# Optimization experiments

Hardware: AMD Instinct MI355X
Metric: run time of the kernel (lower is better)

Reference implementation:

```python
import jax, jax.numpy as jnp
import numpy as np

N_A, N_B = 50000, 10000
E = 300000
IN_F, HID, BEL_OUT, INC_OUT = 256, 256, 128, 128


def _gconv(x_src, W, b, src, dst, n_src, n_dst):
    """DGL GraphConv with norm='both': D_in^{-1/2} A D_out^{-1/2} X W + b, degs clamped to >=1."""
    ones = jnp.ones(src.shape[0], x_src.dtype)
    deg_out = jnp.maximum(jax.ops.segment_sum(ones, src, num_segments=n_src), 1.0)
    deg_in = jnp.maximum(jax.ops.segment_sum(ones, dst, num_segments=n_dst), 1.0)
    h = (x_src * jax.lax.rsqrt(deg_out)[:, None]) @ W        # [n_src, out]
    agg = jax.ops.segment_sum(h[src], dst, num_segments=n_dst)  # scatter-add messages
    return agg * jax.lax.rsqrt(deg_in)[:, None] + b


def setup_inputs() -> dict:
    key = jax.random.key(0)
    ks = jax.random.split(key, 12)
    s = 1.0 / np.sqrt(IN_F)
    sh = 1.0 / np.sqrt(HID)
    return {
        "x_a": jax.random.normal(ks[0], (N_A, IN_F), jnp.float32),
        "x_b": jax.random.normal(ks[1], (N_B, IN_F), jnp.float32),
        "W1_bel": jax.random.normal(ks[2], (IN_F, HID), jnp.float32) * s,
        "b1_bel": jnp.zeros((HID,), jnp.float32),
        "W1_inc": jax.random.normal(ks[3], (IN_F, HID), jnp.float32) * s,
        "b1_inc": jnp.zeros((HID,), jnp.float32),
        "W2_bel": jax.random.normal(ks[4], (HID, BEL_OUT), jnp.float32) * sh,
        "b2_bel": jnp.zeros((BEL_OUT,), jnp.float32),
        "W2_inc": jax.random.normal(ks[5], (HID, INC_OUT), jnp.float32) * sh,
        "b2_inc": jnp.zeros((INC_OUT,), jnp.float32),
        "bel_src": jax.random.randint(ks[6], (E,), 0, N_A, jnp.int32),
        "bel_dst": jax.random.randint(ks[7], (E,), 0, N_B, jnp.int32),
        "inc_src": jax.random.randint(ks[8], (E,), 0, N_B, jnp.int32),
        "inc_dst": jax.random.randint(ks[9], (E,), 0, N_A, jnp.int32),
    }


def reference(x_a, x_b, W1_bel, b1_bel, W1_inc, b1_inc, W2_bel, b2_bel,
              W2_inc, b2_inc, bel_src, bel_dst, inc_src, inc_dst):
    n_a, n_b = x_a.shape[0], x_b.shape[0]
    # layer 1 (HeteroGraphConv, mean over a single relation per dst type = identity)
    h_b = _gconv(x_a, W1_bel, b1_bel, bel_src, bel_dst, n_a, n_b)  # 'belongs_to': A->B
    h_a = _gconv(x_b, W1_inc, b1_inc, inc_src, inc_dst, n_b, n_a)  # 'including' : B->A
    h_a = jax.nn.relu(h_a)
    h_b = jax.nn.relu(h_b)
    # layer 2
    out_b = _gconv(h_a, W2_bel, b2_bel, bel_src, bel_dst, n_a, n_b)  # [N_B, bel_out]
    out_a = _gconv(h_b, W2_inc, b2_inc, inc_src, inc_dst, n_b, n_a)  # [N_A, inc_out]
    return out_a, out_b
```

## Files before the change

kernel.cpp:

```cpp
#include <hip/hip_runtime.h>


#define NA 50000
#define NB 10000
#define NE 300000
#define GB 625
#define HB 1172
#define PB 64
#define CB 300
#define CS 32

typedef unsigned short u16;
typedef unsigned int u32;
typedef __attribute__((ext_vector_type(8))) short short8;
typedef __attribute__((ext_vector_type(4))) float f32x4;
typedef __attribute__((ext_vector_type(2))) float f32x2;
typedef __attribute__((ext_vector_type(4))) unsigned short u16x4;
typedef __attribute__((ext_vector_type(4))) int i32x4;

__device__ __forceinline__ float bf2f(u16 h){
  union { u32 u; float f; } x; x.u = ((u32)h) << 16; return x.f;
}
__device__ __forceinline__ u16 f2bf(float f){
  union { float f; u32 u; } x; x.f = f;
  u32 r = (x.u + 0x7FFFu + ((x.u >> 16) & 1u)) >> 16;
  return (u16)r;
}

__device__ __forceinline__ void pack_elem(int t,
    const float* __restrict__ W1b, const float* __restrict__ W1i,
    const float* __restrict__ W2b, const float* __restrict__ W2i,
    u16* __restrict__ pwh, u16* __restrict__ pwl){
  const float* W; int N; int tt;
  if (t < 65536)       { W = W1b; N = 256; tt = t; }
  else if (t < 131072) { W = W1i; N = 256; tt = t - 65536; }
  else if (t < 163840) { W = W2b; N = 128; tt = t - 131072; }
  else                 { W = W2i; N = 128; tt = t - 163840; }
  int j = tt & 7, lane = (tt >> 3) & 63, tile = tt >> 9;
  int nT = N >> 4;
  int nt = tile % nT, kt = tile / nT;
  int k = kt * 32 + ((lane >> 4) << 3) + j;
  int n = nt * 16 + (lane & 15);
  float v = W[k * N + n];
  u16 hi = f2bf(v);
  pwh[t] = hi;
  pwl[t] = f2bf(v - bf2f(hi));
}

__global__ __launch_bounds__(256) void pre_kernel(
    int* __restrict__ z, int nz4, const float* __restrict__ W1i,
    u16* __restrict__ pwh, u16* __restrict__ pwl){
  int g = blockIdx.x * blockDim.x + threadIdx.x;
  int s = gridDim.x * blockDim.x;
  i32x4* z4 = (i32x4*)z;
  i32x4 zero = {0, 0, 0, 0};
  for (int i = g; i < nz4; i += s) __builtin_nontemporal_store(zero, z4 + i);
  for (int t = g; t < 65536; t += s)
    pack_elem(65536 + t, nullptr, W1i, nullptr, nullptr, pwh, pwl);
}

__device__ __forceinline__ void gemm_dev(int blk, const float* __restrict__ A,
                                         const u16* __restrict__ PWH,
                                         const u16* __restrict__ PWL,
                                         const float* __restrict__ bias,
                                         const float* __restrict__ rs,
                                         float* __restrict__ Cf,
                                         u16* __restrict__ C16,
                                         int M, int nT, int wpsShift,
                                         int doRelu, int ldC, int colOff){
  int wave = blk * 4 + (threadIdx.x >> 6);
  int lane = threadIdx.x & 63;
  int strips = M >> 4;
  int strip = wave >> wpsShift;
  if (strip >= strips) return;
  int slice = wave & ((1 << wpsShift) - 1);
  int ntPer = nT >> wpsShift;
  int ntStart = slice * ntPer;
  int r16 = lane & 15, quad = lane >> 4;
  int m0 = strip << 4;
  const float* aBase = A + (size_t)(m0 + r16) * 256 + quad * 8;
  short8 ah[8], al[8];
#pragma unroll
  for (int kt = 0; kt < 8; ++kt){
    float4 p0 = *(const float4*)(aBase + kt * 32);
    float4 p1 = *(const float4*)(aBase + kt * 32 + 4);
    float v[8] = {p0.x, p0.y, p0.z, p0.w, p1.x, p1.y, p1.z, p1.w};
    short8 h, l;
#pragma unroll
    for (int j = 0; j < 8; ++j){
      u16 hb = f2bf(v[j]);
      h[j] = (short)hb;
      l[j] = (short)f2bf(v[j] - bf2f(hb));
    }
    ah[kt] = h; al[kt] = l;
  }
  float rscale[4];
#pragma unroll
  for (int r = 0; r < 4; ++r) rscale[r] = rs ? rs[m0 + quad * 4 + r] : 1.f;
  for (int nt = ntStart; nt < ntStart + ntPer; ++nt){
    f32x4 acc = {0.f, 0.f, 0.f, 0.f};
    const u16* bh = PWH + ((size_t)nt * 64 + lane) * 8;
    const u16* bl = PWL + ((size_t)nt * 64 + lane) * 8;
#pragma unroll
    for (int kt = 0; kt < 8; ++kt){
      short8 wh = *(const short8*)(bh + (size_t)kt * nT * 512);
      short8 wl = *(const short8*)(bl + (size_t)kt * nT * 512);
      acc = __builtin_amdgcn_mfma_f32_16x16x32_bf16(ah[kt], wh, acc, 0, 0, 0);
      acc = __builtin_amdgcn_mfma_f32_16x16x32_bf16(al[kt], wh, acc, 0, 0, 0);
      acc = __builtin_amdgcn_mfma_f32_16x16x32_bf16(ah[kt], wl, acc, 0, 0, 0);
    }
    int col = nt * 16 + r16;
    float bv = bias ? bias[col] : 0.f;
#pragma unroll
    for (int r = 0; r < 4; ++r){
      float v = acc[r] * rscale[r] + bv;
      if (doRelu) v = fmaxf(v, 0.f);
      size_t o = (size_t)(m0 + quad * 4 + r) * ldC + colOff + col;
      if (C16) __builtin_nontemporal_store(f2bf(v), C16 + o);
      else     __builtin_nontemporal_store(v, Cf + o);
    }
  }
}

__global__ __launch_bounds__(256) void mega_kernel(
    const float* __restrict__ xb,
    const u16* __restrict__ WH1i, const u16* __restrict__ WL1i,
    u16* __restrict__ G12,
    const int* __restrict__ bs, const int* __restrict__ bd,
    const int* __restrict__ isc, const int* __restrict__ idt,
    int* __restrict__ c_bs, int* __restrict__ c_bd,
    int* __restrict__ c_is, int* __restrict__ c_id,
    int* __restrict__ rank_bel, int* __restrict__ rank_inc,
    const float* __restrict__ W1b, const float* __restrict__ W2b,
    const float* __restrict__ W2i,
    u16* __restrict__ pwh, u16* __restrict__ pwl,
    const float* __restrict__ xa, u16* __restrict__ xa16){
  int blk = blockIdx.x;
  if (blk < GB){
    gemm_dev(blk, xb, WH1i, WL1i, nullptr, nullptr,
             nullptr, G12, NB, 16, 2, 0, 384, 0);
  } else if (blk < GB + HB){
    int g = (blk - GB) * blockDim.x + threadIdx.x;
    int s = HB * blockDim.x;
    for (int e = g; e < NE; e += s){
      atomicAdd(&c_bs[bs[e] * CS], 1);
      rank_bel[e] = atomicAdd(&c_bd[bd[e] * CS], 1);
      atomicAdd(&c_is[isc[e] * CS], 1);
      rank_inc[e] = atomicAdd(&c_id[idt[e] * CS], 1);
    }
  } else if (blk < GB + HB + PB){
    int g = (blk - GB - HB) * blockDim.x + threadIdx.x;
    int s = PB * blockDim.x;
    for (int v = g; v < 131072; v += s){
      int t = v < 65536 ? v : v + 65536;
      pack_elem(t, W1b, nullptr, W2b, W2i, pwh, pwl);
    }
  } else {
    int g = ((blk - GB - HB - PB) * blockDim.x + threadIdx.x) * 4;
    int s = CB * blockDim.x * 4;
    for (int i = g; i < NA * 256; i += s){
      float4 v = *(const float4*)(xa + i);
      u16x4 o;
      o.x = f2bf(v.x); o.y = f2bf(v.y); o.z = f2bf(v.z); o.w = f2bf(v.w);
      __builtin_nontemporal_store(o, (u16x4*)(xa16 + i));
    }
  }
}

template<int SEG>
__device__ __forceinline__ void scan_block(const int* __restrict__ cnt,
                                           int* __restrict__ off, int n){
  __shared__ int wsum[16];
  int tid = threadIdx.x, lane = tid & 63, wid = tid >> 6;
  int i0 = tid * SEG;
  int v[SEG];
#pragma unroll
  for (int r = 0; r < SEG; ++r){
    int idx = i0 + r;
    v[r] = (idx < n) ? cnt[idx * CS] : 0;
  }
  int sum = 0;
#pragma unroll
  for (int r = 0; r < SEG; ++r) sum += v[r];
  int x = sum;
#pragma unroll
  for (int d = 1; d < 64; d <<= 1){
    int t = __shfl_up(x, d, 64);
    if (lane >= d) x += t;
  }
  if (lane == 63) wsum[wid] = x;
  __syncthreads();
  if (wid == 0){
    int ws = (lane < 16) ? wsum[lane] : 0;
#pragma unroll
    for (int d = 1; d < 16; d <<= 1){
      int t = __shfl_up(ws, d, 64);
      if (lane >= d) ws += t;
    }
    if (lane < 16) wsum[lane] = ws;
  }
  __syncthreads();
  int run = (wid ? wsum[wid - 1] : 0) + (x - sum);
#pragma unroll
  for (int r = 0; r < SEG; ++r){
    int idx = i0 + r;
    if (idx < n) off[idx] = run;
    run += v[r];
  }
  if (tid == 0) off[n] = wsum[15];
}

__global__ __launch_bounds__(1024) void scan_scales_kernel(
    const int* __restrict__ c_bs, const int* __restrict__ c_bd,
    const int* __restrict__ c_is, const int* __restrict__ c_id,
    int* __restrict__ off_bel, int* __restrict__ off_inc,
    float* __restrict__ s_ob, float* __restrict__ s_ib,
    float* __restrict__ s_oi, float* __restrict__ s_ii){
  if (blockIdx.x >= 2){
    int g = (blockIdx.x - 2) * blockDim.x + threadIdx.x;
    int s = (gridDim.x - 2) * blockDim.x;
    for (int i = g; i < NA; i += s){
      int a = c_bs[i * CS]; s_ob[i] = rsqrtf((float)(a > 1 ? a : 1));
      int b = c_id[i * CS]; s_ii[i] = rsqrtf((float)(b > 1 ? b : 1));
      if (i < NB){
        int c = c_bd[i * CS]; s_ib[i] = rsqrtf((float)(c > 1 ? c : 1));
        int d = c_is[i * CS]; s_oi[i] = rsqrtf((float)(d > 1 ? d : 1));
      }
    }
    return;
  }
  if (blockIdx.x == 0) scan_block<10>(c_bd, off_bel, NB);
  else                 scan_block<49>(c_id, off_inc, NA);
}

__global__ __launch_bounds__(256) void fill_kernel(
    const int* __restrict__ bs, const int* __restrict__ bd,
    const int* __restrict__ isc, const int* __restrict__ idt,
    const int* __restrict__ rank_bel, const int* __restrict__ rank_inc,
    const int* __restrict__ off_bel, const int* __restrict__ off_inc,
    int* __restrict__ csr_bel, int* __restrict__ csr_inc){
  int g = blockIdx.x * blockDim.x + threadIdx.x;
  int s = gridDim.x * blockDim.x;
  for (int e = g; e < NE; e += s){
    csr_bel[off_bel[bd[e]] + rank_bel[e]] = bs[e];
    csr_inc[off_inc[idt[e]] + rank_inc[e]] = isc[e];
  }
}

__global__ __launch_bounds__(256) void agg_bel_kernel(
    const u16* __restrict__ X, const float* __restrict__ ss,
    const int* __restrict__ off, const int* __restrict__ csr,
    float* __restrict__ Pf, int nDst){
  int wave = blockIdx.x * 4 + (threadIdx.x >> 6);
  int lane = threadIdx.x & 63;
  if (wave >= nDst) return;
  int b0 = off[wave], b1 = off[wave + 1];
  int deg = b1 - b0;
  int part = lane >> 5;
  int cl = lane & 31;
  int c = cl * 8;
  float acc[8];
#pragma unroll
  for (int q = 0; q < 8; ++q) acc[q] = 0.f;
  int idx = 0; float sc = 0.f;
  if (lane < deg){
    idx = csr[b0 + lane];
    sc = ss ? ss[idx] : 1.f;
  }
  int lim = deg < 64 ? deg : 64;
  for (int u = 0; u < lim; u += 8){
    const u16* addr[4]; float w[4];
#pragma unroll
    for (int k = 0; k < 4; ++k){
      int e = u + k * 2 + part;
      int t = e < lim ? e : 0;
      int s0 = __shfl(idx, t, 64);
      float c0 = __shfl(sc, t, 64);
      w[k] = e < lim ? c0 : 0.f;
      addr[k] = X + (size_t)s0 * 256 + c;
    }
    short8 v[4];
#pragma unroll
    for (int k = 0; k < 4; ++k) v[k] = *(const short8*)addr[k];
#pragma unroll
    for (int k = 0; k < 4; ++k)
#pragma unroll
      for (int q = 0; q < 8; ++q) acc[q] += bf2f((u16)v[k][q]) * w[k];
  }
  for (int j = b0 + 64 + part; j < b1; j += 2){
    int s0 = csr[j];
    float c0 = ss ? ss[s0] : 1.f;
    short8 v0 = *(const short8*)(X + (size_t)s0 * 256 + c);
#pragma unroll
    for (int q = 0; q < 8; ++q) acc[q] += bf2f((u16)v0[q]) * c0;
  }
#pragma unroll
  for (int q = 0; q < 8; ++q) acc[q] += __shfl_xor(acc[q], 32, 64);
  if (part == 0){
    f32x4 f0 = {acc[0], acc[1], acc[2], acc[3]};
    f32x4 f1 = {acc[4], acc[5], acc[6], acc[7]};
    __builtin_nontemporal_store(f0, (f32x4*)(Pf + (size_t)wave * 256 + c));
    __builtin_nontemporal_store(f1, (f32x4*)(Pf + (size_t)wave * 256 + c + 4));
  }
}

__global__ __launch_bounds__(256) void gemmHG_kernel(
    const float* __restrict__ Pb,
    const u16* __restrict__ WH1b, const u16* __restrict__ WL1b,
    const float* __restrict__ b1b, const float* __restrict__ s_ib,
    const u16* __restrict__ WH2i, const u16* __restrict__ WL2i,
    u16* __restrict__ G12){
  __shared__ float Hs[16][260];
  int w = threadIdx.x >> 6;
  int lane = threadIdx.x & 63;
  int r16 = lane & 15, quad = lane >> 4;
  int m0 = blockIdx.x << 4;
  const float* aBase = Pb + (size_t)(m0 + r16) * 256 + quad * 8;
  short8 ah[8], al[8];
#pragma unroll
  for (int kt = 0; kt < 8; ++kt){
    float4 p0 = *(const float4*)(aBase + kt * 32);
    float4 p1 = *(const float4*)(aBase + kt * 32 + 4);
    float v[8] = {p0.x, p0.y, p0.z, p0.w, p1.x, p1.y, p1.z, p1.w};
    short8 h, l;
#pragma unroll
    for (int j = 0; j < 8; ++j){
      u16 hb = f2bf(v[j]);
      h[j] = (short)hb;
      l[j] = (short)f2bf(v[j] - bf2f(hb));
    }
    ah[kt] = h; al[kt] = l;
  }
  float rs1[4];
#pragma unroll
  for (int r = 0; r < 4; ++r) rs1[r] = s_ib[m0 + quad * 4 + r];
  for (int nt = w * 4; nt < w * 4 + 4; ++nt){
    f32x4 acc = {0.f, 0.f, 0.f, 0.f};
    const u16* bh = WH1b + ((size_t)nt * 64 + lane) * 8;
    const u16* bl = WL1b + ((size_t)nt * 64 + lane) * 8;
#pragma unroll
    for (int kt = 0; kt < 8; ++kt){
      short8 wh = *(const short8*)(bh + (size_t)kt * 16 * 512);
      short8 wl = *(const short8*)(bl + (size_t)kt * 16 * 512);
      acc = __builtin_amdgcn_mfma_f32_16x16x32_bf16(ah[kt], wh, acc, 0, 0, 0);
      acc = __builtin_amdgcn_mfma_f32_16x16x32_bf16(al[kt], wh, acc, 0, 0, 0);
      acc = __builtin_amdgcn_mfma_f32_16x16x32_bf16(ah[kt], wl, acc, 0, 0, 0);
    }
    int col = nt * 16 + r16;
    float bv = b1b[col];
#pragma unroll
    for (int r = 0; r < 4; ++r)
      Hs[quad * 4 + r][col] = fmaxf(acc[r] * rs1[r] + bv, 0.f);
  }
  __syncthreads();
  short8 ah2[8], al2[8];
#pragma unroll
  for (int kt = 0; kt < 8; ++kt){
    float4 p0 = *(const float4*)&Hs[r16][kt * 32 + quad * 8];
    float4 p1 = *(const float4*)&Hs[r16][kt * 32 + quad * 8 + 4];
    float v[8] = {p0.x, p0.y, p0.z, p0.w, p1.x, p1.y, p1.z, p1.w};
    short8 h, l;
#pragma unroll
    for (int j = 0; j < 8; ++j){
      u16 hb = f2bf(v[j]);
      h[j] = (short)hb;
      l[j] = (short)f2bf(v[j] - bf2f(hb));
    }
    ah2[kt] = h; al2[kt] = l;
  }
  for (int nt = w * 2; nt < w * 2 + 2; ++nt){
    f32x4 acc = {0.f, 0.f, 0.f, 0.f};
    const u16* bh = WH2i + ((size_t)nt * 64 + lane) * 8;
    const u16* bl = WL2i + ((size_t)nt * 64 + lane) * 8;
#pragma unroll
    for (int kt = 0; kt < 8; ++kt){
      short8 wh = *(const short8*)(bh + (size_t)kt * 8 * 512);
      short8 wl = *(const short8*)(bl + (size_t)kt * 8 * 512);
      acc = __builtin_amdgcn_mfma_f32_16x16x32_bf16(ah2[kt], wh, acc, 0, 0, 0);
      acc = __builtin_amdgcn_mfma_f32_16x16x32_bf16(al2[kt], wh, acc, 0, 0, 0);
      acc = __builtin_amdgcn_mfma_f32_16x16x32_bf16(ah2[kt], wl, acc, 0, 0, 0);
    }
    int col = nt * 16 + r16;
#pragma unroll
    for (int r = 0; r < 4; ++r){
      u16 o = f2bf(acc[r]);
      __builtin_nontemporal_store(o, G12 + (size_t)(m0 + quad * 4 + r) * 384 + 256 + col);
    }
  }
}

__global__ __launch_bounds__(256) void agg_inc2_kernel(
    const u16* __restrict__ G12, const int* __restrict__ off,
    const int* __restrict__ csr, const float* __restrict__ s_oi,
    const float* __restrict__ s_ii, const float* __restrict__ s_ob,
    const float* __restrict__ b1i, const float* __restrict__ b2i,
    u16* __restrict__ Ha, float* __restrict__ outa){
  int wave = blockIdx.x * 4 + (threadIdx.x >> 6);
  int lane = threadIdx.x & 63;
  if (wave >= NA) return;
  int b0 = off[wave], b1 = off[wave + 1];
  int deg = b1 - b0;
  int c1 = lane * 4;
  int c2 = lane * 2;
  float acc[6];
#pragma unroll
  for (int q = 0; q < 6; ++q) acc[q] = 0.f;
  int idx = 0; float sc = 0.f;
  if (lane < deg){
    idx = csr[b0 + lane];
    sc = s_oi[idx];
  }
  int lim = deg < 64 ? deg : 64;
  for (int u = 0; u < lim; u += 4){
    ushort4 va[4]; ushort2 vb[4]; float w[4];
#pragma unroll
    for (int k = 0; k < 4; ++k){
      int e = u + k;
      int t = e < lim ? e : 0;
      int se = __shfl(idx, t, 64);
      float c0 = __shfl(sc, t, 64);
      w[k] = e < lim ? c0 : 0.f;
      const u16* r = G12 + (size_t)se * 384;
      va[k] = *(const ushort4*)(r + c1);
      vb[k] = *(const ushort2*)(r + 256 + c2);
    }
#pragma unroll
    for (int k = 0; k < 4; ++k){
      acc[0] += bf2f(va[k].x) * w[k];
      acc[1] += bf2f(va[k].y) * w[k];
      acc[2] += bf2f(va[k].z) * w[k];
      acc[3] += bf2f(va[k].w) * w[k];
      acc[4] += bf2f(vb[k].x) * w[k];
      acc[5] += bf2f(vb[k].y) * w[k];
    }
  }
  for (int j = b0 + 64; j < b1; ++j){
    int se = csr[j];
    float c0 = s_oi[se];
    const u16* r = G12 + (size_t)se * 384;
    ushort4 va = *(const ushort4*)(r + c1);
    ushort2 vb = *(const ushort2*)(r + 256 + c2);
    acc[0] += bf2f(va.x) * c0; acc[1] += bf2f(va.y) * c0;
    acc[2] += bf2f(va.z) * c0; acc[3] += bf2f(va.w) * c0;
    acc[4] += bf2f(vb.x) * c0; acc[5] += bf2f(vb.y) * c0;
  }
  float sii = s_ii[wave], sob = s_ob[wave];
  float4 bb1 = *(const float4*)(b1i + c1);
  f32x2 bb2 = *(const f32x2*)(b2i + c2);
  u16x4 o1;
  o1.x = f2bf(fmaxf(acc[0] * sii + bb1.x, 0.f) * sob);
  o1.y = f2bf(fmaxf(acc[1] * sii + bb1.y, 0.f) * sob);
  o1.z = f2bf(fmaxf(acc[2] * sii + bb1.z, 0.f) * sob);
  o1.w = f2bf(fmaxf(acc[3] * sii + bb1.w, 0.f) * sob);
  __builtin_nontemporal_store(o1, (u16x4*)(Ha + (size_t)wave * 256 + c1));
  f32x2 o2 = {acc[4] * sii + bb2.x, acc[5] * sii + bb2.y};
  __builtin_nontemporal_store(o2, (f32x2*)(outa + (size_t)wave * 128 + c2));
}

__global__ __launch_bounds__(256) void gemm_kernel(
    const float* __restrict__ A,
    const u16* __restrict__ PWH, const u16* __restrict__ PWL,
    const float* __restrict__ bias, const float* __restrict__ rs,
    float* __restrict__ Cf, u16* __restrict__ C16,
    int M, int nT, int wpsShift, int doRelu, int ldC, int colOff){
  gemm_dev(blockIdx.x, A, PWH, PWL, bias, rs, Cf, C16,
           M, nT, wpsShift, doRelu, ldC, colOff);
}

extern "C" void kernel_launch(void* const* d_in, const int* in_sizes, int n_in,
                              void* d_out, int out_size, void* d_ws, size_t ws_size,
                              hipStream_t stream){
  const float* x_a = (const float*)d_in[0];
  const float* x_b = (const float*)d_in[1];
  const float* W1b = (const float*)d_in[2];
  const float* b1b = (const float*)d_in[3];
  const float* W1i = (const float*)d_in[4];
  const float* b1i = (const float*)d_in[5];
  const float* W2b = (const float*)d_in[6];
  const float* b2b = (const float*)d_in[7];
  const float* W2i = (const float*)d_in[8];
  const float* b2i = (const float*)d_in[9];
  const int* bs  = (const int*)d_in[10];
  const int* bd  = (const int*)d_in[11];
  const int* isc = (const int*)d_in[12];
  const int* idt = (const int*)d_in[13];

  char* w = (char*)d_ws;
  size_t o = 0;
  auto take = [&](size_t bytes) -> void* {
    void* p = w + o; o = (o + bytes + 255) & ~(size_t)255; return p;
  };
  int* zint = (int*)take((size_t)120000 * CS * sizeof(int));
  int* c_bs = zint;
  int* c_bd = zint + (size_t)50000 * CS;
  int* c_is = zint + (size_t)60000 * CS;
  int* c_id = zint + (size_t)70000 * CS;
  int* rank_bel = (int*)take(NE * sizeof(int));
  int* rank_inc = (int*)take(NE * sizeof(int));
  int* off_bel = (int*)take((NB + 1) * sizeof(int));
  int* off_inc = (int*)take((NA + 1) * sizeof(int));
  int* csr_bel = (int*)take(NE * sizeof(int));
  int* csr_inc = (int*)take(NE * sizeof(int));
  float* s_ob = (float*)take(NA * sizeof(float));
  float* s_ib = (float*)take(NB * sizeof(float));
  float* s_oi = (float*)take(NB * sizeof(float));
  float* s_ii = (float*)take(NA * sizeof(float));
  u16* pwh = (u16*)take(196608 * sizeof(u16));
  u16* pwl = (u16*)take(196608 * sizeof(u16));
  u16* pwh1b = pwh, *pwh1i = pwh + 65536, *pwh2b = pwh + 131072, *pwh2i = pwh + 163840;
  u16* pwl1b = pwl, *pwl1i = pwl + 65536, *pwl2b = pwl + 131072, *pwl2i = pwl + 163840;
  u16* xa16 = (u16*)take((size_t)NA * 256 * sizeof(u16));
  u16* G12  = (u16*)take((size_t)NB * 384 * sizeof(u16));
  u16* H_a  = (u16*)take((size_t)NA * 256 * sizeof(u16));
  float* P_b = (float*)take((size_t)NB * 256 * sizeof(float));

  float* out_a = (float*)d_out;
  float* out_b = (float*)d_out + (size_t)NA * 128;

  pre_kernel<<<512, 256, 0, stream>>>(zint, 120000 * CS / 4, W1i, pwh, pwl);
  mega_kernel<<<GB + HB + PB + CB, 256, 0, stream>>>(
      x_b, pwh1i, pwl1i, G12,
      bs, bd, isc, idt, c_bs, c_bd, c_is, c_id, rank_bel, rank_inc,
      W1b, W2b, W2i, pwh, pwl, x_a, xa16);
  scan_scales_kernel<<<52, 1024, 0, stream>>>(c_bs, c_bd, c_is, c_id,
                                              off_bel, off_inc,
                                              s_ob, s_ib, s_oi, s_ii);
  fill_kernel<<<1172, 256, 0, stream>>>(bs, bd, isc, idt, rank_bel, rank_inc,
                                        off_bel, off_inc, csr_bel, csr_inc);
  agg_bel_kernel<<<2500, 256, 0, stream>>>(xa16, s_ob, off_bel, csr_bel, P_b, NB);
  gemmHG_kernel<<<625, 256, 0, stream>>>(P_b, pwh1b, pwl1b, b1b, s_ib,
                                         pwh2i, pwl2i, G12);
  agg_inc2_kernel<<<12500, 256, 0, stream>>>(G12, off_inc, csr_inc, s_oi,
                                             s_ii, s_ob, b1i, b2i, H_a, out_a);
  agg_bel_kernel<<<2500, 256, 0, stream>>>(H_a, nullptr, off_bel, csr_bel, P_b, NB);
  gemm_kernel<<<625, 256, 0, stream>>>(P_b, pwh2b, pwl2b, b2b, s_ib,
                                       out_b, nullptr, NB, 8, 2, 0, 128, 0);
}
```

Measured before the change: 401.0 us.

## Replace padded degree counters with compact and 4-way split counters

Drops the 32-int padding per degree counter, which had each counter sit on its own cache line, so the zeroing pass and the counter reads touch far less memory. For the small node sets (10k B nodes), the counters become four sub-counters per node picked by edge index, which spreads atomic contention, and the scan runs over 40000 entries so CSR offsets still stay correct. The large sets use dense unpadded counters. Denser counters risk more same-line atomic contention, and the bel scan now does more work per thread.

New measurement: 363.5 us. 9.4% less time.

```diff
diff --git a/kernel.cpp b/kernel.cpp
--- a/kernel.cpp
+++ b/kernel.cpp
@@ -8,7 +8,6 @@
 #define HB 1172
 #define PB 64
 #define CB 300
-#define CS 32
 
 typedef unsigned short u16;
 typedef unsigned int u32;
@@ -128,8 +127,8 @@
     u16* __restrict__ G12,
     const int* __restrict__ bs, const int* __restrict__ bd,
     const int* __restrict__ isc, const int* __restrict__ idt,
-    int* __restrict__ c_bs, int* __restrict__ c_bd,
-    int* __restrict__ c_is, int* __restrict__ c_id,
+    int* __restrict__ c_bs, int* __restrict__ c_bd4,
+    int* __restrict__ c_is4, int* __restrict__ c_id,
     int* __restrict__ rank_bel, int* __restrict__ rank_inc,
     const float* __restrict__ W1b, const float* __restrict__ W2b,
     const float* __restrict__ W2i,
@@ -143,10 +142,11 @@
     int g = (blk - GB) * blockDim.x + threadIdx.x;
     int s = HB * blockDim.x;
     for (int e = g; e < NE; e += s){
-      atomicAdd(&c_bs[bs[e] * CS], 1);
-      rank_bel[e] = atomicAdd(&c_bd[bd[e] * CS], 1);
-      atomicAdd(&c_is[isc[e] * CS], 1);
-      rank_inc[e] = atomicAdd(&c_id[idt[e] * CS], 1);
+      int r = e & 3;
+      atomicAdd(&c_bs[bs[e]], 1);
+      rank_bel[e] = atomicAdd(&c_bd4[bd[e] * 4 + r], 1);
+      atomicAdd(&c_is4[isc[e] * 4 + r], 1);
+      rank_inc[e] = atomicAdd(&c_id[idt[e]], 1);
     }
   } else if (blk < GB + HB + PB){
     int g = (blk - GB - HB) * blockDim.x + threadIdx.x;
@@ -177,7 +177,7 @@
 #pragma unroll
   for (int r = 0; r < SEG; ++r){
     int idx = i0 + r;
-    v[r] = (idx < n) ? cnt[idx * CS] : 0;
+    v[r] = (idx < n) ? cnt[idx] : 0;
   }
   int sum = 0;
 #pragma unroll
@@ -211,25 +211,29 @@
 }
 
 __global__ __launch_bounds__(1024) void scan_scales_kernel(
-    const int* __restrict__ c_bs, const int* __restrict__ c_bd,
-    const int* __restrict__ c_is, const int* __restrict__ c_id,
-    int* __restrict__ off_bel, int* __restrict__ off_inc,
+    const int* __restrict__ c_bs, const int* __restrict__ c_bd4,
+    const int* __restrict__ c_is4, const int* __restrict__ c_id,
+    int* __restrict__ off_bel4, int* __restrict__ off_inc,
     float* __restrict__ s_ob, float* __restrict__ s_ib,
     float* __restrict__ s_oi, float* __restrict__ s_ii){
   if (blockIdx.x >= 2){
     int g = (blockIdx.x - 2) * blockDim.x + threadIdx.x;
     int s = (gridDim.x - 2) * blockDim.x;
     for (int i = g; i < NA; i += s){
-      int a = c_bs[i * CS]; s_ob[i] = rsqrtf((float)(a > 1 ? a : 1));
-      int b = c_id[i * CS]; s_ii[i] = rsqrtf((float)(b > 1 ? b : 1));
+      int a = c_bs[i]; s_ob[i] = rsqrtf((float)(a > 1 ? a : 1));
+      int b = c_id[i]; s_ii[i] = rsqrtf((float)(b > 1 ? b : 1));
       if (i < NB){
-        int c = c_bd[i * CS]; s_ib[i] = rsqrtf((float)(c > 1 ? c : 1));
-        int d = c_is[i * CS]; s_oi[i] = rsqrtf((float)(d > 1 ? d : 1));
+        i32x4 cb = *(const i32x4*)(c_bd4 + i * 4);
+        int c = cb[0] + cb[1] + cb[2] + cb[3];
+        s_ib[i] = rsqrtf((float)(c > 1 ? c : 1));
+        i32x4 ci = *(const i32x4*)(c_is4 + i * 4);
+        int d = ci[0] + ci[1] + ci[2] + ci[3];
+        s_oi[i] = rsqrtf((float)(d > 1 ? d : 1));
       }
     }
     return;
   }
-  if (blockIdx.x == 0) scan_block<10>(c_bd, off_bel, NB);
+  if (blockIdx.x == 0) scan_block<40>(c_bd4, off_bel4, 40000);
   else                 scan_block<49>(c_id, off_inc, NA);
 }
 
@@ -237,24 +241,25 @@
     const int* __restrict__ bs, const int* __restrict__ bd,
     const int* __restrict__ isc, const int* __restrict__ idt,
     const int* __restrict__ rank_bel, const int* __restrict__ rank_inc,
-    const int* __restrict__ off_bel, const int* __restrict__ off_inc,
+    const int* __restrict__ off_bel4, const int* __restrict__ off_inc,
     int* __restrict__ csr_bel, int* __restrict__ csr_inc){
   int g = blockIdx.x * blockDim.x + threadIdx.x;
   int s = gridDim.x * blockDim.x;
   for (int e = g; e < NE; e += s){
-    csr_bel[off_bel[bd[e]] + rank_bel[e]] = bs[e];
+    int r = e & 3;
+    csr_bel[off_bel4[bd[e] * 4 + r] + rank_bel[e]] = bs[e];
     csr_inc[off_inc[idt[e]] + rank_inc[e]] = isc[e];
   }
 }
 
 __global__ __launch_bounds__(256) void agg_bel_kernel(
     const u16* __restrict__ X, const float* __restrict__ ss,
-    const int* __restrict__ off, const int* __restrict__ csr,
+    const int* __restrict__ off4, const int* __restrict__ csr,
     float* __restrict__ Pf, int nDst){
   int wave = blockIdx.x * 4 + (threadIdx.x >> 6);
   int lane = threadIdx.x & 63;
   if (wave >= nDst) return;
-  int b0 = off[wave], b1 = off[wave + 1];
+  int b0 = off4[wave * 4], b1 = off4[wave * 4 + 4];
   int deg = b1 - b0;
   int part = lane >> 5;
   int cl = lane & 31;
@@ -490,15 +495,15 @@
   auto take = [&](size_t bytes) -> void* {
     void* p = w + o; o = (o + bytes + 255) & ~(size_t)255; return p;
   };
-  int* zint = (int*)take((size_t)120000 * CS * sizeof(int));
-  int* c_bs = zint;
-  int* c_bd = zint + (size_t)50000 * CS;
-  int* c_is = zint + (size_t)60000 * CS;
-  int* c_id = zint + (size_t)70000 * CS;
+  int* zint = (int*)take((size_t)180000 * sizeof(int));
+  int* c_bs  = zint;
+  int* c_bd4 = zint + 50000;
+  int* c_is4 = zint + 90000;
+  int* c_id  = zint + 130000;
   int* rank_bel = (int*)take(NE * sizeof(int));
   int* rank_inc = (int*)take(NE * sizeof(int));
-  int* off_bel = (int*)take((NB + 1) * sizeof(int));
-  int* off_inc = (int*)take((NA + 1) * sizeof(int));
+  int* off_bel4 = (int*)take((40000 + 1) * sizeof(int));
+  int* off_inc  = (int*)take((NA + 1) * sizeof(int));
   int* csr_bel = (int*)take(NE * sizeof(int));
   int* csr_inc = (int*)take(NE * sizeof(int));
   float* s_ob = (float*)take(NA * sizeof(float));
@@ -517,22 +522,22 @@
   float* out_a = (float*)d_out;
   float* out_b = (float*)d_out + (size_t)NA * 128;
 
-  pre_kernel<<<512, 256, 0, stream>>>(zint, 120000 * CS / 4, W1i, pwh, pwl);
+  pre_kernel<<<256, 256, 0, stream>>>(zint, 180000 / 4, W1i, pwh, pwl);
   mega_kernel<<<GB + HB + PB + CB, 256, 0, stream>>>(
       x_b, pwh1i, pwl1i, G12,
-      bs, bd, isc, idt, c_bs, c_bd, c_is, c_id, rank_bel, rank_inc,
+      bs, bd, isc, idt, c_bs, c_bd4, c_is4, c_id, rank_bel, rank_inc,
       W1b, W2b, W2i, pwh, pwl, x_a, xa16);
-  scan_scales_kernel<<<52, 1024, 0, stream>>>(c_bs, c_bd, c_is, c_id,
-                                              off_bel, off_inc,
+  scan_scales_kernel<<<52, 1024, 0, stream>>>(c_bs, c_bd4, c_is4, c_id,
+                                              off_bel4, off_inc,
                                               s_ob, s_ib, s_oi, s_ii);
   fill_kernel<<<1172, 256, 0, stream>>>(bs, bd, isc, idt, rank_bel, rank_inc,
-                                        off_bel, off_inc, csr_bel, csr_inc);
-  agg_bel_kernel<<<2500, 256, 0, stream>>>(xa16, s_ob, off_bel, csr_bel, P_b, NB);
+                                        off_bel4, off_inc, csr_bel, csr_inc);
+  agg_bel_kernel<<<2500, 256, 0, stream>>>(xa16, s_ob, off_bel4, csr_bel, P_b, NB);
   gemmHG_kernel<<<625, 256, 0, stream>>>(P_b, pwh1b, pwl1b, b1b, s_ib,
                                          pwh2i, pwl2i, G12);
   agg_inc2_kernel<<<12500, 256, 0, stream>>>(G12, off_inc, csr_inc, s_oi,
                                              s_ii, s_ob, b1i, b2i, H_a, out_a);
-  agg_bel_kernel<<<2500, 256, 0, stream>>>(H_a, nullptr, off_bel, csr_bel, P_b, NB);
+  agg_bel_kernel<<<2500, 256, 0, stream>>>(H_a, nullptr, off_bel4, csr_bel, P_b, NB);
   gemm_kernel<<<625, 256, 0, stream>>>(P_b, pwh2b, pwl2b, b2b, s_ib,
                                        out_b, nullptr, NB, 8, 2, 0, 128, 0);
 }
```

## Replace global atomic degree counting with bin-partitioned LDS histograms

Applied to the files above, without the earlier changes.

Degree counting and CSR fill now use per-block shared-memory histograms. Each block owns a contiguous range of bins and scans the whole edge array, counting only edges whose endpoint falls in its range. Counts are written directly, so the padded counters, their zeroing pass and the per-edge rank arrays are no longer needed. Global atomics are replaced by LDS atomics, but each block now rereads all edges: 16x per array for counting and 32x per array in the fill, across only 64 blocks. With so few blocks the CSR fill may also be less parallel than before.

Result: slower. 709.3 us (+76.9%).

```diff
diff --git a/kernel.cpp b/kernel.cpp
--- a/kernel.cpp
+++ b/kernel.cpp
@@ -5,10 +5,9 @@
 #define NB 10000
 #define NE 300000
 #define GB 625
-#define HB 1172
+#define HBIN 64
 #define PB 64
 #define CB 300
-#define CS 32
 
 typedef unsigned short u16;
 typedef unsigned int u32;
@@ -48,13 +47,10 @@
 }
 
 __global__ __launch_bounds__(256) void pre_kernel(
-    int* __restrict__ z, int nz4, const float* __restrict__ W1i,
+    const float* __restrict__ W1i,
     u16* __restrict__ pwh, u16* __restrict__ pwl){
   int g = blockIdx.x * blockDim.x + threadIdx.x;
   int s = gridDim.x * blockDim.x;
-  i32x4* z4 = (i32x4*)z;
-  i32x4 zero = {0, 0, 0, 0};
-  for (int i = g; i < nz4; i += s) __builtin_nontemporal_store(zero, z4 + i);
   for (int t = g; t < 65536; t += s)
     pack_elem(65536 + t, nullptr, W1i, nullptr, nullptr, pwh, pwl);
 }
@@ -130,33 +126,48 @@
     const int* __restrict__ isc, const int* __restrict__ idt,
     int* __restrict__ c_bs, int* __restrict__ c_bd,
     int* __restrict__ c_is, int* __restrict__ c_id,
-    int* __restrict__ rank_bel, int* __restrict__ rank_inc,
     const float* __restrict__ W1b, const float* __restrict__ W2b,
     const float* __restrict__ W2i,
     u16* __restrict__ pwh, u16* __restrict__ pwl,
     const float* __restrict__ xa, u16* __restrict__ xa16){
+  __shared__ int lcnt[3136];
   int blk = blockIdx.x;
   if (blk < GB){
     gemm_dev(blk, xb, WH1i, WL1i, nullptr, nullptr,
              nullptr, G12, NB, 16, 2, 0, 384, 0);
-  } else if (blk < GB + HB){
-    int g = (blk - GB) * blockDim.x + threadIdx.x;
-    int s = HB * blockDim.x;
-    for (int e = g; e < NE; e += s){
-      atomicAdd(&c_bs[bs[e] * CS], 1);
-      rank_bel[e] = atomicAdd(&c_bd[bd[e] * CS], 1);
-      atomicAdd(&c_is[isc[e] * CS], 1);
-      rank_inc[e] = atomicAdd(&c_id[idt[e] * CS], 1);
-    }
-  } else if (blk < GB + HB + PB){
-    int g = (blk - GB - HB) * blockDim.x + threadIdx.x;
+  } else if (blk < GB + HBIN){
+    int h = blk - GB;
+    int sub = h >> 4, b16 = h & 15;
+    const int* src; int nbins; int* dst;
+    if (sub == 0)      { src = bs;  nbins = NA; dst = c_bs; }
+    else if (sub == 1) { src = bd;  nbins = NB; dst = c_bd; }
+    else if (sub == 2) { src = isc; nbins = NB; dst = c_is; }
+    else               { src = idt; nbins = NA; dst = c_id; }
+    int binsPer = nbins >> 4;
+    int lo = b16 * binsPer;
+    for (int i = threadIdx.x; i < binsPer; i += 256) lcnt[i] = 0;
+    __syncthreads();
+    const i32x4* s4 = (const i32x4*)src;
+    for (int i = threadIdx.x; i < NE / 4; i += 256){
+      i32x4 v = s4[i];
+#pragma unroll
+      for (int k = 0; k < 4; ++k){
+        int d = v[k] - lo;
+        if ((unsigned)d < (unsigned)binsPer) atomicAdd(&lcnt[d], 1);
+      }
+    }
+    __syncthreads();
+    for (int i = threadIdx.x; i < binsPer; i += 256)
+      dst[lo + i] = lcnt[i];
+  } else if (blk < GB + HBIN + PB){
+    int g = (blk - GB - HBIN) * blockDim.x + threadIdx.x;
     int s = PB * blockDim.x;
     for (int v = g; v < 131072; v += s){
       int t = v < 65536 ? v : v + 65536;
       pack_elem(t, W1b, nullptr, W2b, W2i, pwh, pwl);
     }
   } else {
-    int g = ((blk - GB - HB - PB) * blockDim.x + threadIdx.x) * 4;
+    int g = ((blk - GB - HBIN - PB) * blockDim.x + threadIdx.x) * 4;
     int s = CB * blockDim.x * 4;
     for (int i = g; i < NA * 256; i += s){
       float4 v = *(const float4*)(xa + i);
@@ -165,49 +176,6 @@
       __builtin_nontemporal_store(o, (u16x4*)(xa16 + i));
     }
   }
-}
-
-template<int SEG>
-__device__ __forceinline__ void scan_block(const int* __restrict__ cnt,
-                                           int* __restrict__ off, int n){
-  __shared__ int wsum[16];
-  int tid = threadIdx.x, lane = tid & 63, wid = tid >> 6;
-  int i0 = tid * SEG;
-  int v[SEG];
-#pragma unroll
-  for (int r = 0; r < SEG; ++r){
-    int idx = i0 + r;
-    v[r] = (idx < n) ? cnt[idx * CS] : 0;
-  }
-  int sum = 0;
-#pragma unroll
-  for (int r = 0; r < SEG; ++r) sum += v[r];
-  int x = sum;
-#pragma unroll
-  for (int d = 1; d < 64; d <<= 1){
-    int t = __shfl_up(x, d, 64);
-    if (lane >= d) x += t;
-  }
-  if (lane == 63) wsum[wid] = x;
-  __syncthreads();
-  if (wid == 0){
-    int ws = (lane < 16) ? wsum[lane] : 0;
-#pragma unroll
-    for (int d = 1; d < 16; d <<= 1){
-      int t = __shfl_up(ws, d, 64);
-      if (lane >= d) ws += t;
-    }
-    if (lane < 16) wsum[lane] = ws;
-  }
-  __syncthreads();
-  int run = (wid ? wsum[wid - 1] : 0) + (x - sum);
-#pragma unroll
-  for (int r = 0; r < SEG; ++r){
-    int idx = i0 + r;
-    if (idx < n) off[idx] = run;
-    run += v[r];
-  }
-  if (tid == 0) off[n] = wsum[15];
 }
 
 __global__ __launch_bounds__(1024) void scan_scales_kernel(
@@ -220,30 +188,115 @@
     int g = (blockIdx.x - 2) * blockDim.x + threadIdx.x;
     int s = (gridDim.x - 2) * blockDim.x;
     for (int i = g; i < NA; i += s){
-      int a = c_bs[i * CS]; s_ob[i] = rsqrtf((float)(a > 1 ? a : 1));
-      int b = c_id[i * CS]; s_ii[i] = rsqrtf((float)(b > 1 ? b : 1));
+      int a = c_bs[i]; s_ob[i] = rsqrtf((float)(a > 1 ? a : 1));
+      int b = c_id[i]; s_ii[i] = rsqrtf((float)(b > 1 ? b : 1));
       if (i < NB){
-        int c = c_bd[i * CS]; s_ib[i] = rsqrtf((float)(c > 1 ? c : 1));
-        int d = c_is[i * CS]; s_oi[i] = rsqrtf((float)(d > 1 ? d : 1));
+        int c = c_bd[i]; s_ib[i] = rsqrtf((float)(c > 1 ? c : 1));
+        int d = c_is[i]; s_oi[i] = rsqrtf((float)(d > 1 ? d : 1));
       }
     }
     return;
   }
-  if (blockIdx.x == 0) scan_block<10>(c_bd, off_bel, NB);
-  else                 scan_block<49>(c_id, off_inc, NA);
+  __shared__ int wsum[16];
+  int tid = threadIdx.x, lane = tid & 63, wid = tid >> 6;
+  if (blockIdx.x == 0){
+    const int SEG = 10;
+    int i0 = tid * SEG;
+    int v[SEG];
+#pragma unroll
+    for (int r = 0; r < SEG; ++r){
+      int idx = i0 + r;
+      v[r] = (idx < NB) ? c_bd[idx] : 0;
+    }
+    int sum = 0;
+#pragma unroll
+    for (int r = 0; r < SEG; ++r) sum += v[r];
+    int x = sum;
+#pragma unroll
+    for (int d = 1; d < 64; d <<= 1){
+      int t = __shfl_up(x, d, 64);
+      if (lane >= d) x += t;
+    }
+    if (lane == 63) wsum[wid] = x;
+    __syncthreads();
+    if (wid == 0){
+      int ws = (lane < 16) ? wsum[lane] : 0;
+#pragma unroll
+      for (int d = 1; d < 16; d <<= 1){
+        int t = __shfl_up(ws, d, 64);
+        if (lane >= d) ws += t;
+      }
+      if (lane < 16) wsum[lane] = ws;
+    }
+    __syncthreads();
+    int run = (wid ? wsum[wid - 1] : 0) + (x - sum);
+#pragma unroll
+    for (int r = 0; r < SEG; ++r){
+      int idx = i0 + r;
+      if (idx < NB) off_bel[idx] = run;
+      run += v[r];
+    }
+    if (tid == 0) off_bel[NB] = wsum[15];
+  } else {
+    const int n = NA;
+    int seg = (n + 1023) >> 10;
+    int i0 = tid * seg;
+    int lim = i0 + seg; if (lim > n) lim = n;
+    int sum = 0;
+    for (int i = i0; i < lim; ++i) sum += c_id[i];
+    int x = sum;
+#pragma unroll
+    for (int d = 1; d < 64; d <<= 1){
+      int t = __shfl_up(x, d, 64);
+      if (lane >= d) x += t;
+    }
+    if (lane == 63) wsum[wid] = x;
+    __syncthreads();
+    if (wid == 0){
+      int ws = (lane < 16) ? wsum[lane] : 0;
+#pragma unroll
+      for (int d = 1; d < 16; d <<= 1){
+        int t = __shfl_up(ws, d, 64);
+        if (lane >= d) ws += t;
+      }
+      if (lane < 16) wsum[lane] = ws;
+    }
+    __syncthreads();
+    int run = (wid ? wsum[wid - 1] : 0) + (x - sum);
+    for (int i = i0; i < lim; ++i){ off_inc[i] = run; run += c_id[i]; }
+    if (tid == 0) off_inc[n] = wsum[15];
+  }
 }
 
 __global__ __launch_bounds__(256) void fill_kernel(
     const int* __restrict__ bs, const int* __restrict__ bd,
     const int* __restrict__ isc, const int* __restrict__ idt,
-    const int* __restrict__ rank_bel, const int* __restrict__ rank_inc,
     const int* __restrict__ off_bel, const int* __restrict__ off_inc,
     int* __restrict__ csr_bel, int* __restrict__ csr_inc){
-  int g = blockIdx.x * blockDim.x + threadIdx.x;
-  int s = gridDim.x * blockDim.x;
-  for (int e = g; e < NE; e += s){
-    csr_bel[off_bel[bd[e]] + rank_bel[e]] = bs[e];
-    csr_inc[off_inc[idt[e]] + rank_inc[e]] = isc[e];
+  __shared__ int lrank[1568];
+  int sub = blockIdx.x >> 5, b32 = blockIdx.x & 31;
+  const int* dsts; const int* vals; const int* off; int* csr; int nbins;
+  if (sub == 0){ dsts = bd;  vals = bs;  off = off_bel; csr = csr_bel; nbins = NB; }
+  else         { dsts = idt; vals = isc; off = off_inc; csr = csr_inc; nbins = NA; }
+  int binsPer = (nbins + 31) >> 5;
+  int lo = b32 * binsPer;
+  int hi = lo + binsPer; if (hi > nbins) hi = nbins;
+  int nb = hi - lo;
+  for (int i = threadIdx.x; i < nb; i += 256) lrank[i] = 0;
+  __syncthreads();
+  const i32x4* d4 = (const i32x4*)dsts;
+  const i32x4* v4 = (const i32x4*)vals;
+  for (int i = threadIdx.x; i < NE / 4; i += 256){
+    i32x4 d = d4[i];
+    i32x4 v = v4[i];
+#pragma unroll
+    for (int k = 0; k < 4; ++k){
+      int b = d[k] - lo;
+      if ((unsigned)b < (unsigned)nb){
+        int r = atomicAdd(&lrank[b], 1);
+        csr[off[d[k]] + r] = v[k];
+      }
+    }
   }
 }
 
@@ -490,13 +543,10 @@
   auto take = [&](size_t bytes) -> void* {
     void* p = w + o; o = (o + bytes + 255) & ~(size_t)255; return p;
   };
-  int* zint = (int*)take((size_t)120000 * CS * sizeof(int));
-  int* c_bs = zint;
-  int* c_bd = zint + (size_t)50000 * CS;
-  int* c_is = zint + (size_t)60000 * CS;
-  int* c_id = zint + (size_t)70000 * CS;
-  int* rank_bel = (int*)take(NE * sizeof(int));
-  int* rank_inc = (int*)take(NE * sizeof(int));
+  int* c_bs = (int*)take(NA * sizeof(int));
+  int* c_bd = (int*)take(NB * sizeof(int));
+  int* c_is = (int*)take(NB * sizeof(int));
+  int* c_id = (int*)take(NA * sizeof(int));
   int* off_bel = (int*)take((NB + 1) * sizeof(int));
   int* off_inc = (int*)take((NA + 1) * sizeof(int));
   int* csr_bel = (int*)take(NE * sizeof(int));
@@ -517,16 +567,16 @@
   float* out_a = (float*)d_out;
   float* out_b = (float*)d_out + (size_t)NA * 128;
 
-  pre_kernel<<<512, 256, 0, stream>>>(zint, 120000 * CS / 4, W1i, pwh, pwl);
-  mega_kernel<<<GB + HB + PB + CB, 256, 0, stream>>>(
+  pre_kernel<<<128, 256, 0, stream>>>(W1i, pwh, pwl);
+  mega_kernel<<<GB + HBIN + PB + CB, 256, 0, stream>>>(
       x_b, pwh1i, pwl1i, G12,
-      bs, bd, isc, idt, c_bs, c_bd, c_is, c_id, rank_bel, rank_inc,
+      bs, bd, isc, idt, c_bs, c_bd, c_is, c_id,
       W1b, W2b, W2i, pwh, pwl, x_a, xa16);
   scan_scales_kernel<<<52, 1024, 0, stream>>>(c_bs, c_bd, c_is, c_id,
                                               off_bel, off_inc,
                                               s_ob, s_ib, s_oi, s_ii);
-  fill_kernel<<<1172, 256, 0, stream>>>(bs, bd, isc, idt, rank_bel, rank_inc,
-                                        off_bel, off_inc, csr_bel, csr_inc);
+  fill_kernel<<<64, 256, 0, stream>>>(bs, bd, isc, idt,
+                                      off_bel, off_inc, csr_bel, csr_inc);
   agg_bel_kernel<<<2500, 256, 0, stream>>>(xa16, s_ob, off_bel, csr_bel, P_b, NB);
   gemmHG_kernel<<<625, 256, 0, stream>>>(P_b, pwh1b, pwl1b, b1b, s_ib,
                                          pwh2i, pwl2i, G12);
```
